# Performance work log

Hardware: AMD Instinct MI355X
Metric: run time of the kernel (lower is better)

Reference implementation:

```python
import jax, jax.numpy as jnp
import numpy as np

K = 10  # knn_graph default neighbors (self excluded)
NEG = 0.2  # LeakyReLU slope


def lrelu(x):
    return jnp.where(x > 0, x, NEG * x)


def conv1x1_1d(x, w):  # x: (B,Ci,N), w: (Co,Ci)
    return jnp.einsum('oi,bin->bon', w, x)


def conv1x1_2d(x, w):  # x: (B,Ci,N,k), w: (Co,Ci)
    return jnp.einsum('oi,bink->bonk', w, x)


def bn1(x, s, b):  # folded eval-mode BN, x: (B,C,N)
    return x * s[None, :, None] + b[None, :, None]


def bn2(x, s, b):  # x: (B,C,N,k)
    return x * s[None, :, None, None] + b[None, :, None, None]


def knn_graph(x, k=K):
    # x: (B, D, N) -> edge features (B, 2D, N, k)
    xt = jnp.transpose(x, (0, 2, 1))  # (B,N,D)
    sq = jnp.sum(xt * xt, axis=-1)  # (B,N)
    d2 = sq[:, :, None] + sq[:, None, :] - 2.0 * jnp.einsum('bnd,bmd->bnm', xt, xt)
    _, idx = jax.lax.top_k(-d2, k + 1)  # nearest k+1 incl. self
    idx = idx[:, :, 1:]  # drop self -> (B,N,k)
    B = xt.shape[0]
    feats = xt[jnp.arange(B)[:, None, None], idx]  # (B,N,k,D)
    center = xt[:, :, None, :]  # (B,N,1,D)
    edge = jnp.concatenate((feats - center, jnp.broadcast_to(center, feats.shape)), axis=-1)
    return jnp.transpose(edge, (0, 3, 1, 2))  # (B,2D,N,k)


def _make_params(key):
    ks = iter(jax.random.split(key, 32))
    def W(co, ci):
        return jax.random.normal(next(ks), (co, ci), jnp.float32) * (1.0 / np.sqrt(ci))
    def SB(c):
        return (jax.random.uniform(next(ks), (c,), jnp.float32, 0.5, 1.5),
                jax.random.normal(next(ks), (c,), jnp.float32) * 0.1)
    p = {}
    p['w1'] = W(64, 6);    p['s1'], p['b1'] = SB(64)
    p['w2'] = W(64, 64);   p['s2'], p['b2'] = SB(64)
    p['w3'] = W(64, 128);  p['s3'], p['b3'] = SB(64)
    p['w4'] = W(64, 64);   p['s4'], p['b4'] = SB(64)
    p['w5'] = W(64, 128);  p['s5'], p['b5'] = SB(64)
    p['w6'] = W(1024, 192); p['s6'], p['b6'] = SB(1024)
    p['w7'] = W(64, 16);   p['s7'], p['b7'] = SB(64)
    p['wp1'] = W(256, 1280); p['sp1'], p['bp1'] = SB(256)
    p['wp2'] = W(256, 256);  p['sp2'], p['bp2'] = SB(256)
    p['wp3'] = W(128, 256);  p['sp3'], p['bp3'] = SB(128)
    p['wp4'] = W(6, 128)
    return p


def setup_inputs() -> dict:
    key = jax.random.key(0)
    k0, k1, k2 = jax.random.split(key, 3)
    inp = {
        'points': jax.random.normal(k0, (8, 2048, 3), jnp.float32),
        'label': jax.random.uniform(k1, (8, 16), jnp.float32),
    }
    inp.update(_make_params(k2))
    return inp


def reference(points, label,
              w1, s1, b1, w2, s2, b2, w3, s3, b3, w4, s4, b4, w5, s5, b5,
              w6, s6, b6, w7, s7, b7,
              wp1, sp1, bp1, wp2, sp2, bp2, wp3, sp3, bp3, wp4):
    B, N, _ = points.shape
    x0 = jnp.transpose(points, (0, 2, 1))  # (B,3,N)

    e1 = knn_graph(x0)                                   # (B,6,N,k)
    h = lrelu(bn2(conv1x1_2d(e1, w1), s1, b1))
    out1 = jnp.max(lrelu(bn2(conv1x1_2d(h, w2), s2, b2)), axis=-1)  # (B,64,N)

    e2 = knn_graph(out1)                                 # (B,128,N,k)
    h = lrelu(bn2(conv1x1_2d(e2, w3), s3, b3))
    out2 = jnp.max(lrelu(bn2(conv1x1_2d(h, w4), s4, b4)), axis=-1)  # (B,64,N)

    e3 = knn_graph(out2)                                 # (B,128,N,k)
    out3 = jnp.max(lrelu(bn2(conv1x1_2d(e3, w5), s5, b5)), axis=-1)  # (B,64,N)

    comb = jnp.concatenate((out1, out2, out3), axis=1)   # (B,192,N)
    out4 = lrelu(bn1(conv1x1_1d(comb, w6), s6, b6))      # (B,1024,N)
    out4 = jnp.max(out4, axis=-1, keepdims=True)         # (B,1024,1)

    cat_vet = lrelu(bn1(conv1x1_1d(label[:, :, None], w7), s7, b7))  # (B,64,1)
    glob = jnp.broadcast_to(jnp.concatenate((out4, cat_vet), axis=1), (B, 1088, N))

    out = jnp.concatenate((out1, out2, out3, glob), axis=1)  # (B,1280,N)
    out = lrelu(bn1(conv1x1_1d(out, wp1), sp1, bp1))
    out = lrelu(bn1(conv1x1_1d(out, wp2), sp2, bp2))  # dropout = identity (eval)
    out = lrelu(bn1(conv1x1_1d(out, wp3), sp3, bp3))
    out = conv1x1_1d(out, wp4)                         # (B,6,N)
    return jnp.transpose(out, (0, 2, 1))               # (B,N,6)
```

## Files before the change

### kernel.cpp

```cpp
#include <hip/hip_runtime.h>
#include <float.h>

#define NEG 0.2f
constexpr int BATCH = 8;
constexpr int NPTS  = 2048;
constexpr int KNN   = 10;
constexpr int KP1   = 11;

__device__ __forceinline__ float lrelu(float x) { return x > 0.f ? x : NEG * x; }

__device__ __forceinline__ unsigned long long dkey(float d, int m) {
    unsigned u = __float_as_uint(d);
    u ^= (unsigned)((int)u >> 31) | 0x80000000u;
    return ((unsigned long long)u << 32) | (unsigned)m;
}

template<int D>
__global__ void sq_kernel(const float* __restrict__ xt, float* __restrict__ sq) {
    int i = blockIdx.x * 256 + threadIdx.x;
    if (i >= BATCH * NPTS) return;
    const float* p = xt + (size_t)i * D;
    float s = 0.f;
    #pragma unroll
    for (int d = 0; d < D; ++d) s += p[d] * p[d];
    sq[i] = s;
}

__global__ void sq64_kernel(const float* __restrict__ xt, float* __restrict__ sq) {
    int i = blockIdx.x * 256 + threadIdx.x;
    if (i >= BATCH * NPTS) return;
    const float4* p = (const float4*)(xt + (size_t)i * 64);
    float4 s4 = {0.f, 0.f, 0.f, 0.f};
    #pragma unroll
    for (int d = 0; d < 16; ++d) {
        float4 v = p[d];
        s4.x += v.x * v.x; s4.y += v.y * v.y; s4.z += v.z * v.z; s4.w += v.w * v.w;
    }
    sq[i] = (s4.x + s4.y) + (s4.z + s4.w);
}

template<int D>
__global__ __launch_bounds__(256) void knn_kernel(const float* __restrict__ xt,
                                                  const float* __restrict__ sq,
                                                  int* __restrict__ idx_out) {
    const int bn = blockIdx.x;
    const int b  = bn / NPTS;
    const int tid = threadIdx.x;

    __shared__ float xq[D];
    for (int i = tid; i < D; i += 256) xq[i] = xt[(size_t)bn * D + i];
    __syncthreads();

    const float sqn = sq[bn];
    const float* xb = xt + (size_t)b * NPTS * D;

    unsigned long long lk[KP1];
    #pragma unroll
    for (int j = 0; j < KP1; ++j) lk[j] = ~0ULL;

    for (int m = tid; m < NPTS; m += 256) {
        const float* xm = xb + (size_t)m * D;
        float dot = 0.f;
        #pragma unroll
        for (int i = 0; i < D; ++i) dot += xq[i] * xm[i];
        float cd = sqn + sq[b * NPTS + m] - 2.f * dot;
        unsigned long long key = dkey(cd, m);
        if (key < lk[KP1 - 1]) {
            #pragma unroll
            for (int j = 0; j < KP1; ++j) {
                bool better = key < lk[j];
                unsigned long long tk = lk[j];
                if (better) { lk[j] = key; key = tk; }
            }
        }
    }

    __shared__ unsigned long long sk[256 * KP1];
    #pragma unroll
    for (int j = 0; j < KP1; ++j) sk[tid * KP1 + j] = lk[j];
    __syncthreads();

    for (int step = 1; step < 256; step <<= 1) {
        if ((tid & (2 * step - 1)) == 0) {
            unsigned long long* ka = sk + tid * KP1;
            unsigned long long* kb = sk + (tid + step) * KP1;
            unsigned long long rk[KP1];
            int pa = 0, pb = 0;
            #pragma unroll
            for (int j = 0; j < KP1; ++j) {
                unsigned long long av = ka[pa], bv = kb[pb];
                bool takeA = av < bv;
                if (takeA) { rk[j] = av; ++pa; } else { rk[j] = bv; ++pb; }
            }
            #pragma unroll
            for (int j = 0; j < KP1; ++j) ka[j] = rk[j];
        }
        __syncthreads();
    }

    if (tid < KNN) idx_out[(size_t)bn * KNN + tid] = (int)(unsigned)(sk[tid + 1]);
}

__global__ __launch_bounds__(256) void knn64_kernel(const float* __restrict__ xt,
                                                    const float* __restrict__ sq,
                                                    int* __restrict__ idx_out) {
    const int t  = threadIdx.x;
    const int qg = t >> 5;
    const int lc = t & 31;
    const int bn0 = blockIdx.x * 8;
    const int bn  = bn0 + qg;
    const int b   = bn >> 11;
    const float* xb = xt + (size_t)b * NPTS * 64;

    __shared__ __align__(16) char smem[22528];
    float4 (*tile4)[16] = reinterpret_cast<float4(*)[16]>(smem);
    unsigned long long* sk = reinterpret_cast<unsigned long long*>(smem);

    float4 xq[16];
    {
        const float4* xqp = (const float4*)(xt + (size_t)bn * 64);
        #pragma unroll
        for (int i = 0; i < 16; ++i) xq[i] = xqp[i];
    }
    const float sqn = sq[bn];
    const float* sqb_ = sq + b * NPTS;

    unsigned long long lk[KP1];
    #pragma unroll
    for (int j = 0; j < KP1; ++j) lk[j] = ~0ULL;

    const int ci  = t >> 3;
    const int sub = t & 7;

    for (int t0 = 0; t0 < NPTS; t0 += 32) {
        __syncthreads();
        {
            const float4* src = (const float4*)(xb + (size_t)(t0 + ci) * 64 + sub * 8);
            float4 u0 = src[0], u1 = src[1];
            tile4[ci][(2 * sub)     ^ (ci & 15)] = u0;
            tile4[ci][(2 * sub + 1) ^ (ci & 15)] = u1;
        }
        __syncthreads();

        const int m = t0 + lc;
        float a0 = 0.f, a1 = 0.f, a2 = 0.f, a3 = 0.f;
        #pragma unroll
        for (int i = 0; i < 16; ++i) {
            float4 v = tile4[lc][i ^ (lc & 15)];
            a0 += xq[i].x * v.x;
            a1 += xq[i].y * v.y;
            a2 += xq[i].z * v.z;
            a3 += xq[i].w * v.w;
        }
        float dot = (a0 + a1) + (a2 + a3);
        float cd = sqn + sqb_[m] - 2.f * dot;
        unsigned long long key = dkey(cd, m);
        if (key < lk[KP1 - 1]) {
            #pragma unroll
            for (int j = 0; j < KP1; ++j) {
                bool better = key < lk[j];
                unsigned long long tk = lk[j];
                if (better) { lk[j] = key; key = tk; }
            }
        }
    }

    __syncthreads();
    #pragma unroll
    for (int j = 0; j < KP1; ++j) sk[t * KP1 + j] = lk[j];
    __syncthreads();

    for (int step = 1; step < 32; step <<= 1) {
        if ((lc & (2 * step - 1)) == 0) {
            unsigned long long* ka = sk + t * KP1;
            unsigned long long* kb = sk + (t + step) * KP1;
            unsigned long long rk[KP1];
            int pa = 0, pb = 0;
            #pragma unroll
            for (int j = 0; j < KP1; ++j) {
                unsigned long long av = ka[pa], bv = kb[pb];
                bool takeA = av < bv;
                if (takeA) { rk[j] = av; ++pa; } else { rk[j] = bv; ++pb; }
            }
            #pragma unroll
            for (int j = 0; j < KP1; ++j) ka[j] = rk[j];
        }
        __syncthreads();
    }

    if (lc < KNN) idx_out[(size_t)bn * KNN + lc] = (int)(unsigned)(sk[(qg * 32) * KP1 + lc + 1]);
}

__global__ __launch_bounds__(64) void edgeconv1_kernel(
    const float* __restrict__ pts, const int* __restrict__ idx,
    const float* __restrict__ w1, const float* __restrict__ s1, const float* __restrict__ b1,
    const float* __restrict__ w2, const float* __restrict__ s2, const float* __restrict__ b2,
    float* __restrict__ outt) {
    const int bn = blockIdx.x;
    const int b  = bn / NPTS;
    const int c  = threadIdx.x;

    const float cx = pts[bn * 3 + 0], cy = pts[bn * 3 + 1], cz = pts[bn * 3 + 2];

    float w1r[6];
    #pragma unroll
    for (int i = 0; i < 6; ++i) w1r[i] = w1[c * 6 + i];
    const float s1c = s1[c], b1c = b1[c], s2c = s2[c], b2c = b2[c];

    __shared__ float h1all[KNN][64];
    #pragma unroll
    for (int k = 0; k < KNN; ++k) {
        const int m = idx[bn * KNN + k];
        const float* f = pts + ((size_t)b * NPTS + m) * 3;
        const float e0 = f[0] - cx, e1 = f[1] - cy, e2 = f[2] - cz;
        float a = w1r[0] * e0 + w1r[1] * e1 + w1r[2] * e2
                + w1r[3] * cx + w1r[4] * cy + w1r[5] * cz;
        h1all[k][c] = lrelu(a * s1c + b1c);
    }
    __syncthreads();

    float a2[KNN];
    #pragma unroll
    for (int k = 0; k < KNN; ++k) a2[k] = 0.f;
    for (int j4 = 0; j4 < 16; ++j4) {
        float4 wv = *(const float4*)&w2[c * 64 + j4 * 4];
        #pragma unroll
        for (int k = 0; k < KNN; ++k) {
            float4 h4 = *(const float4*)&h1all[k][j4 * 4];
            a2[k] += wv.x * h4.x + wv.y * h4.y + wv.z * h4.z + wv.w * h4.w;
        }
    }
    float mx = -FLT_MAX;
    #pragma unroll
    for (int k = 0; k < KNN; ++k) mx = fmaxf(mx, lrelu(a2[k] * s2c + b2c));
    outt[(size_t)bn * 64 + c] = mx;
}

__global__ __launch_bounds__(64) void edgeconv2_kernel(
    const float* __restrict__ xin, const int* __restrict__ idx,
    const float* __restrict__ w3, const float* __restrict__ s3, const float* __restrict__ b3,
    const float* __restrict__ w4, const float* __restrict__ s4, const float* __restrict__ b4,
    float* __restrict__ outt) {
    const int bn = blockIdx.x;
    const int b  = bn / NPTS;
    const int c  = threadIdx.x;

    __shared__ float cen[64];
    __shared__ float fea[KNN][64];
    __shared__ float h1all[KNN][64];
    cen[c] = xin[(size_t)bn * 64 + c];
    #pragma unroll
    for (int k = 0; k < KNN; ++k) {
        const int m = idx[bn * KNN + k];
        fea[k][c] = xin[((size_t)b * NPTS + m) * 64 + c];
    }
    __syncthreads();

    float a[KNN];
    #pragma unroll
    for (int k = 0; k < KNN; ++k) a[k] = 0.f;
    float4 ab = {0.f, 0.f, 0.f, 0.f};
    for (int j4 = 0; j4 < 16; ++j4) {
        float4 wa = *(const float4*)&w3[c * 128 + j4 * 4];
        float4 wb = *(const float4*)&w3[c * 128 + 64 + j4 * 4];
        float4 c4 = *(const float4*)&cen[j4 * 4];
        ab.x += (wb.x - wa.x) * c4.x; ab.y += (wb.y - wa.y) * c4.y;
        ab.z += (wb.z - wa.z) * c4.z; ab.w += (wb.w - wa.w) * c4.w;
        #pragma unroll
        for (int k = 0; k < KNN; ++k) {
            float4 f4 = *(const float4*)&fea[k][j4 * 4];
            a[k] += wa.x * f4.x + wa.y * f4.y + wa.z * f4.z + wa.w * f4.w;
        }
    }
    const float abase = (ab.x + ab.y) + (ab.z + ab.w);
    const float s3c = s3[c], b3c = b3[c], s4c = s4[c], b4c = b4[c];
    #pragma unroll
    for (int k = 0; k < KNN; ++k) h1all[k][c] = lrelu((a[k] + abase) * s3c + b3c);
    __syncthreads();

    float a2[KNN];
    #pragma unroll
    for (int k = 0; k < KNN; ++k) a2[k] = 0.f;
    for (int j4 = 0; j4 < 16; ++j4) {
        float4 wv = *(const float4*)&w4[c * 64 + j4 * 4];
        #pragma unroll
        for (int k = 0; k < KNN; ++k) {
            float4 h4 = *(const float4*)&h1all[k][j4 * 4];
            a2[k] += wv.x * h4.x + wv.y * h4.y + wv.z * h4.z + wv.w * h4.w;
        }
    }
    float mx = -FLT_MAX;
    #pragma unroll
    for (int k = 0; k < KNN; ++k) mx = fmaxf(mx, lrelu(a2[k] * s4c + b4c));
    outt[(size_t)bn * 64 + c] = mx;
}

__global__ __launch_bounds__(64) void edgeconv3_kernel(
    const float* __restrict__ xin, const int* __restrict__ idx,
    const float* __restrict__ w5, const float* __restrict__ s5, const float* __restrict__ b5,
    float* __restrict__ outt) {
    const int bn = blockIdx.x;
    const int b  = bn / NPTS;
    const int c  = threadIdx.x;

    __shared__ float cen[64];
    __shared__ float fea[KNN][64];
    cen[c] = xin[(size_t)bn * 64 + c];
    #pragma unroll
    for (int k = 0; k < KNN; ++k) {
        const int m = idx[bn * KNN + k];
        fea[k][c] = xin[((size_t)b * NPTS + m) * 64 + c];
    }
    __syncthreads();

    float a[KNN];
    #pragma unroll
    for (int k = 0; k < KNN; ++k) a[k] = 0.f;
    float4 ab = {0.f, 0.f, 0.f, 0.f};
    for (int j4 = 0; j4 < 16; ++j4) {
        float4 wa = *(const float4*)&w5[c * 128 + j4 * 4];
        float4 wb = *(const float4*)&w5[c * 128 + 64 + j4 * 4];
        float4 c4 = *(const float4*)&cen[j4 * 4];
        ab.x += (wb.x - wa.x) * c4.x; ab.y += (wb.y - wa.y) * c4.y;
        ab.z += (wb.z - wa.z) * c4.z; ab.w += (wb.w - wa.w) * c4.w;
        #pragma unroll
        for (int k = 0; k < KNN; ++k) {
            float4 f4 = *(const float4*)&fea[k][j4 * 4];
            a[k] += wa.x * f4.x + wa.y * f4.y + wa.z * f4.z + wa.w * f4.w;
        }
    }
    const float abase = (ab.x + ab.y) + (ab.z + ab.w);
    const float s5c = s5[c], b5c = b5[c];
    float mx = -FLT_MAX;
    #pragma unroll
    for (int k = 0; k < KNN; ++k) mx = fmaxf(mx, lrelu((a[k] + abase) * s5c + b5c));
    outt[(size_t)bn * 64 + c] = mx;
}

__global__ __launch_bounds__(64) void catvet_kernel(
    const float* __restrict__ label,
    const float* __restrict__ w7, const float* __restrict__ s7, const float* __restrict__ b7,
    float* __restrict__ catv) {
    const int b = blockIdx.x, c = threadIdx.x;
    float a = 0.f;
    #pragma unroll
    for (int i = 0; i < 16; ++i) a += w7[c * 16 + i] * label[b * 16 + i];
    catv[b * 64 + c] = lrelu(a * s7[c] + b7[c]);
}

__global__ void w6t_kernel(const float* __restrict__ w6, float* __restrict__ w6t) {
    int i = blockIdx.x * 256 + threadIdx.x;
    if (i >= 192 * 1024) return;
    int k = i >> 10, c = i & 1023;
    w6t[i] = w6[c * 192 + k];
}

constexpr int OPTS = 32;
__global__ __launch_bounds__(256) void out4max_kernel(
    const float* __restrict__ out1t, const float* __restrict__ out2t, const float* __restrict__ out3t,
    const float* __restrict__ w6t, float* __restrict__ partial) {
    const int blk = blockIdx.x;
    const int b   = blk >> 6;
    const int nt  = blk & 63;
    const int t   = threadIdx.x;

    __shared__ float xs[192 * OPTS];
    for (int idx = t; idx < 192 * OPTS; idx += 256) {
        int p = idx / 192, r = idx - p * 192;
        const size_t gp = (size_t)b * NPTS + nt * OPTS + p;
        float val;
        if (r < 64)       val = out1t[gp * 64 + r];
        else if (r < 128) val = out2t[gp * 64 + (r - 64)];
        else              val = out3t[gp * 64 + (r - 128)];
        xs[r * OPTS + p] = val;
    }
    __syncthreads();

    float mx0 = -FLT_MAX, mx1 = -FLT_MAX, mx2 = -FLT_MAX, mx3 = -FLT_MAX;
    #pragma unroll
    for (int pg = 0; pg < OPTS / 16; ++pg) {
        float acc0[16], acc1[16], acc2[16], acc3[16];
        #pragma unroll
        for (int p = 0; p < 16; ++p) { acc0[p] = 0.f; acc1[p] = 0.f; acc2[p] = 0.f; acc3[p] = 0.f; }
        #pragma unroll 2
        for (int k = 0; k < 192; ++k) {
            float4 wv = *(const float4*)&w6t[(size_t)k * 1024 + t * 4];
            const float4* xr4 = (const float4*)&xs[k * OPTS + pg * 16];
            #pragma unroll
            for (int p4 = 0; p4 < 4; ++p4) {
                float4 xv = xr4[p4];
                acc0[p4 * 4 + 0] += wv.x * xv.x; acc0[p4 * 4 + 1] += wv.x * xv.y;
                acc0[p4 * 4 + 2] += wv.x * xv.z; acc0[p4 * 4 + 3] += wv.x * xv.w;
                acc1[p4 * 4 + 0] += wv.y * xv.x; acc1[p4 * 4 + 1] += wv.y * xv.y;
                acc1[p4 * 4 + 2] += wv.y * xv.z; acc1[p4 * 4 + 3] += wv.y * xv.w;
                acc2[p4 * 4 + 0] += wv.z * xv.x; acc2[p4 * 4 + 1] += wv.z * xv.y;
                acc2[p4 * 4 + 2] += wv.z * xv.z; acc2[p4 * 4 + 3] += wv.z * xv.w;
                acc3[p4 * 4 + 0] += wv.w * xv.x; acc3[p4 * 4 + 1] += wv.w * xv.y;
                acc3[p4 * 4 + 2] += wv.w * xv.z; acc3[p4 * 4 + 3] += wv.w * xv.w;
            }
        }
        #pragma unroll
        for (int p = 0; p < 16; ++p) {
            mx0 = fmaxf(mx0, acc0[p]); mx1 = fmaxf(mx1, acc1[p]);
            mx2 = fmaxf(mx2, acc2[p]); mx3 = fmaxf(mx3, acc3[p]);
        }
    }
    float4 o = {mx0, mx1, mx2, mx3};
    *(float4*)&partial[(size_t)blk * 1024 + t * 4] = o;
}

__global__ __launch_bounds__(256) void out4reduce_kernel(
    const float* __restrict__ partial,
    const float* __restrict__ s6, const float* __restrict__ b6,
    float* __restrict__ out4m) {
    const int i = blockIdx.x * 256 + threadIdx.x;
    const int b = i >> 10, c = i & 1023;
    float m = -FLT_MAX;
    for (int nt = 0; nt < 64; ++nt)
        m = fmaxf(m, partial[((size_t)b * 64 + nt) * 1024 + c]);
    out4m[i] = lrelu(m * s6[c] + b6[c]);
}

__global__ __launch_bounds__(256) void gbias_kernel(
    const float* __restrict__ out4m, const float* __restrict__ catv,
    const float* __restrict__ wp1, float* __restrict__ g) {
    const int b = blockIdx.x, t = threadIdx.x;
    __shared__ float v[1088];
    for (int i = t; i < 1088; i += 256)
        v[i] = (i < 1024) ? out4m[(size_t)b * 1024 + i] : catv[(size_t)b * 64 + (i - 1024)];
    __syncthreads();
    const float* w = wp1 + (size_t)t * 1280 + 192;
    float4 s4 = {0.f, 0.f, 0.f, 0.f};
    for (int i = 0; i < 272; ++i) {
        float4 wv = *(const float4*)&w[i * 4];
        float4 vv = *(const float4*)&v[i * 4];
        s4.x += wv.x * vv.x; s4.y += wv.y * vv.y; s4.z += wv.z * vv.z; s4.w += wv.w * vv.w;
    }
    g[(size_t)b * 256 + t] = (s4.x + s4.y) + (s4.z + s4.w);
}

constexpr int HP = 16;
constexpr int KC = 16;

__global__ __launch_bounds__(256) void head_kernel(
    const float* __restrict__ out1t, const float* __restrict__ out2t, const float* __restrict__ out3t,
    const float* __restrict__ g,
    const float* __restrict__ wp1, const float* __restrict__ sp1, const float* __restrict__ bp1,
    const float* __restrict__ wp2, const float* __restrict__ sp2, const float* __restrict__ bp2,
    const float* __restrict__ wp3, const float* __restrict__ sp3, const float* __restrict__ bp3,
    const float* __restrict__ wp4, float* __restrict__ out) {
    const int p0 = blockIdx.x * HP;
    const int b  = p0 >> 11;
    const int t  = threadIdx.x;

    __shared__ float smA[4096];
    __shared__ float smB[4096];
    __shared__ float smW[KC * 256];

    for (int e = t; e < 192 * HP; e += 256) {
        int p = e / 192, k = e - p * 192;
        float val;
        if (k < 64)       val = out1t[((size_t)(p0 + p)) * 64 + k];
        else if (k < 128) val = out2t[((size_t)(p0 + p)) * 64 + (k - 64)];
        else              val = out3t[((size_t)(p0 + p)) * 64 + (k - 128)];
        smA[k * HP + p] = val;
    }

    const int og = t & 31;
    const int pg = t >> 5;

    float acc[2][8];
    #pragma unroll
    for (int i = 0; i < 8; ++i) {
        float gv = g[(size_t)b * 256 + og * 8 + i];
        acc[0][i] = gv; acc[1][i] = gv;
    }
    for (int kc = 0; kc < 192 / KC; ++kc) {
        __syncthreads();
        #pragma unroll
        for (int it = 0; it < KC; ++it)
            smW[it * 256 + t] = wp1[(size_t)t * 1280 + kc * KC + it];
        __syncthreads();
        #pragma unroll 4
        for (int kk = 0; kk < KC; ++kk) {
            int k = kc * KC + kk;
            float2 xv = *(const float2*)&smA[k * HP + pg * 2];
            float4 w0 = *(const float4*)&smW[kk * 256 + og * 8];
            float4 w1v = *(const float4*)&smW[kk * 256 + og * 8 + 4];
            float wv[8] = {w0.x, w0.y, w0.z, w0.w, w1v.x, w1v.y, w1v.z, w1v.w};
            #pragma unroll
            for (int i = 0; i < 8; ++i) {
                acc[0][i] += xv.x * wv[i];
                acc[1][i] += xv.y * wv[i];
            }
        }
    }
    #pragma unroll
    for (int i = 0; i < 8; ++i) {
        int o = og * 8 + i;
        float sc = sp1[o], bc = bp1[o];
        smB[o * HP + pg * 2 + 0] = lrelu(acc[0][i] * sc + bc);
        smB[o * HP + pg * 2 + 1] = lrelu(acc[1][i] * sc + bc);
    }

    float acc2[2][8];
    #pragma unroll
    for (int i = 0; i < 8; ++i) { acc2[0][i] = 0.f; acc2[1][i] = 0.f; }
    for (int kc = 0; kc < 256 / KC; ++kc) {
        __syncthreads();
        #pragma unroll
        for (int it = 0; it < KC; ++it)
            smW[it * 256 + t] = wp2[(size_t)t * 256 + kc * KC + it];
        __syncthreads();
        #pragma unroll 4
        for (int kk = 0; kk < KC; ++kk) {
            int k = kc * KC + kk;
            float2 xv = *(const float2*)&smB[k * HP + pg * 2];
            float4 w0 = *(const float4*)&smW[kk * 256 + og * 8];
            float4 w1v = *(const float4*)&smW[kk * 256 + og * 8 + 4];
            float wv[8] = {w0.x, w0.y, w0.z, w0.w, w1v.x, w1v.y, w1v.z, w1v.w};
            #pragma unroll
            for (int i = 0; i < 8; ++i) {
                acc2[0][i] += xv.x * wv[i];
                acc2[1][i] += xv.y * wv[i];
            }
        }
    }
    __syncthreads();
    #pragma unroll
    for (int i = 0; i < 8; ++i) {
        int o = og * 8 + i;
        float sc = sp2[o], bc = bp2[o];
        smA[o * HP + pg * 2 + 0] = lrelu(acc2[0][i] * sc + bc);
        smA[o * HP + pg * 2 + 1] = lrelu(acc2[1][i] * sc + bc);
    }

    const int og3 = t & 15;
    const int p3  = t >> 4;
    float acc3[8];
    #pragma unroll
    for (int i = 0; i < 8; ++i) acc3[i] = 0.f;
    for (int kc = 0; kc < 256 / KC; ++kc) {
        __syncthreads();
        for (int e = t; e < KC * 128; e += 256) {
            int kk = e >> 7, o = e & 127;
            smW[kk * 128 + o] = wp3[(size_t)o * 256 + kc * KC + kk];
        }
        __syncthreads();
        #pragma unroll 4
        for (int kk = 0; kk < KC; ++kk) {
            int k = kc * KC + kk;
            float xv = smA[k * HP + p3];
            float4 w0 = *(const float4*)&smW[kk * 128 + og3 * 8];
            float4 w1v = *(const float4*)&smW[kk * 128 + og3 * 8 + 4];
            float wv[8] = {w0.x, w0.y, w0.z, w0.w, w1v.x, w1v.y, w1v.z, w1v.w};
            #pragma unroll
            for (int i = 0; i < 8; ++i) acc3[i] += xv * wv[i];
        }
    }
    __syncthreads();
    #pragma unroll
    for (int i = 0; i < 8; ++i) {
        int o = og3 * 8 + i;
        float sc = sp3[o], bc = bp3[o];
        smB[o * HP + p3] = lrelu(acc3[i] * sc + bc);
    }
    __syncthreads();

    if (t < HP * 6) {
        int p = t / 6, o = t - p * 6;
        float4 s4 = {0.f, 0.f, 0.f, 0.f};
        for (int k4 = 0; k4 < 32; ++k4) {
            float4 wv = *(const float4*)&wp4[o * 128 + k4 * 4];
            s4.x += wv.x * smB[(k4 * 4 + 0) * HP + p];
            s4.y += wv.y * smB[(k4 * 4 + 1) * HP + p];
            s4.z += wv.z * smB[(k4 * 4 + 2) * HP + p];
            s4.w += wv.w * smB[(k4 * 4 + 3) * HP + p];
        }
        out[((size_t)(p0 + p)) * 6 + o] = (s4.x + s4.y) + (s4.z + s4.w);
    }
}

extern "C" void kernel_launch(void* const* d_in, const int* in_sizes, int n_in,
                              void* d_out, int out_size, void* d_ws, size_t ws_size,
                              hipStream_t stream) {
    const float* points = (const float*)d_in[0];
    const float* label  = (const float*)d_in[1];
    const float* w1  = (const float*)d_in[2];
    const float* s1  = (const float*)d_in[3];
    const float* b1  = (const float*)d_in[4];
    const float* w2  = (const float*)d_in[5];
    const float* s2  = (const float*)d_in[6];
    const float* b2  = (const float*)d_in[7];
    const float* w3  = (const float*)d_in[8];
    const float* s3  = (const float*)d_in[9];
    const float* b3  = (const float*)d_in[10];
    const float* w4  = (const float*)d_in[11];
    const float* s4  = (const float*)d_in[12];
    const float* b4  = (const float*)d_in[13];
    const float* w5  = (const float*)d_in[14];
    const float* s5  = (const float*)d_in[15];
    const float* b5  = (const float*)d_in[16];
    const float* w6  = (const float*)d_in[17];
    const float* s6  = (const float*)d_in[18];
    const float* b6  = (const float*)d_in[19];
    const float* w7  = (const float*)d_in[20];
    const float* s7  = (const float*)d_in[21];
    const float* b7  = (const float*)d_in[22];
    const float* wp1 = (const float*)d_in[23];
    const float* sp1 = (const float*)d_in[24];
    const float* bp1 = (const float*)d_in[25];
    const float* wp2 = (const float*)d_in[26];
    const float* sp2 = (const float*)d_in[27];
    const float* bp2 = (const float*)d_in[28];
    const float* wp3 = (const float*)d_in[29];
    const float* sp3 = (const float*)d_in[30];
    const float* bp3 = (const float*)d_in[31];
    const float* wp4 = (const float*)d_in[32];

    float* ws = (float*)d_ws;
    size_t off = 0;
    auto alloc = [&](size_t nf) { float* p = ws + off; off += nf; return p; };
    float* out1t = alloc((size_t)BATCH * NPTS * 64);
    float* out2t = alloc((size_t)BATCH * NPTS * 64);
    float* out3t = alloc((size_t)BATCH * NPTS * 64);
    float* sqb   = alloc((size_t)BATCH * NPTS);
    float* out4m = alloc((size_t)BATCH * 1024);
    float* catv  = alloc((size_t)BATCH * 64);
    float* gb    = alloc((size_t)BATCH * 256);
    float* w6t   = alloc((size_t)192 * 1024);
    float* part  = alloc((size_t)512 * 1024);
    int* idx1 = (int*)alloc((size_t)BATCH * NPTS * KNN);
    int* idx2 = (int*)alloc((size_t)BATCH * NPTS * KNN);
    int* idx3 = (int*)alloc((size_t)BATCH * NPTS * KNN);

    const int BN = BATCH * NPTS;
    const int sqBlocks = (BN + 255) / 256;

    sq_kernel<3><<<sqBlocks, 256, 0, stream>>>(points, sqb);
    knn_kernel<3><<<BN, 256, 0, stream>>>(points, sqb, idx1);
    edgeconv1_kernel<<<BN, 64, 0, stream>>>(points, idx1, w1, s1, b1, w2, s2, b2, out1t);

    sq64_kernel<<<sqBlocks, 256, 0, stream>>>(out1t, sqb);
    knn64_kernel<<<BN / 8, 256, 0, stream>>>(out1t, sqb, idx2);
    edgeconv2_kernel<<<BN, 64, 0, stream>>>(out1t, idx2, w3, s3, b3, w4, s4, b4, out2t);

    sq64_kernel<<<sqBlocks, 256, 0, stream>>>(out2t, sqb);
    knn64_kernel<<<BN / 8, 256, 0, stream>>>(out2t, sqb, idx3);
    edgeconv3_kernel<<<BN, 64, 0, stream>>>(out2t, idx3, w5, s5, b5, out3t);

    catvet_kernel<<<BATCH, 64, 0, stream>>>(label, w7, s7, b7, catv);
    w6t_kernel<<<(192 * 1024 + 255) / 256, 256, 0, stream>>>(w6, w6t);
    out4max_kernel<<<512, 256, 0, stream>>>(out1t, out2t, out3t, w6t, part);
    out4reduce_kernel<<<BATCH * 1024 / 256, 256, 0, stream>>>(part, s6, b6, out4m);
    gbias_kernel<<<BATCH, 256, 0, stream>>>(out4m, catv, wp1, gb);

    head_kernel<<<BN / HP, 256, 0, stream>>>(out1t, out2t, out3t, gb,
                                             wp1, sp1, bp1, wp2, sp2, bp2, wp3, sp3, bp3,
                                             wp4, (float*)d_out);
}
```

Measured before the change: 1.154 ms.

## Replace shared-memory merge trees in kNN with wavefront shuffle top-k selection

The 3-D kNN kernel now runs one 64-lane wavefront per query instead of 256 threads, and the final top-k selection in both kNN kernels uses repeated shuffle-xor min reductions instead of a shared-memory pairwise merge tree with block barriers. Each of the 11 rounds finds the global minimum key and pops it from the owning lane's sorted list. This removes the large shared-memory buffer and the many __syncthreads, and it frees LDS in knn64 for higher occupancy. In exchange each lane scans more candidates in the 3-D kernel, and every round adds 64-bit shuffle reductions.

```diff
diff --git a/kernel.cpp b/kernel.cpp
--- a/kernel.cpp
+++ b/kernel.cpp
@@ -39,31 +39,30 @@
     sq[i] = (s4.x + s4.y) + (s4.z + s4.w);
 }
 
-template<int D>
-__global__ __launch_bounds__(256) void knn_kernel(const float* __restrict__ xt,
+__global__ __launch_bounds__(64) void knn3_kernel(const float* __restrict__ xt,
                                                   const float* __restrict__ sq,
                                                   int* __restrict__ idx_out) {
     const int bn = blockIdx.x;
-    const int b  = bn / NPTS;
-    const int tid = threadIdx.x;
-
-    __shared__ float xq[D];
-    for (int i = tid; i < D; i += 256) xq[i] = xt[(size_t)bn * D + i];
-    __syncthreads();
-
+    const int b  = bn >> 11;
+    const int l  = threadIdx.x;
+
+    const float qx = xt[(size_t)bn * 3 + 0];
+    const float qy = xt[(size_t)bn * 3 + 1];
+    const float qz = xt[(size_t)bn * 3 + 2];
     const float sqn = sq[bn];
-    const float* xb = xt + (size_t)b * NPTS * D;
+    const float* xb  = xt + (size_t)b * NPTS * 3;
+    const float* sqb_ = sq + (size_t)b * NPTS;
 
     unsigned long long lk[KP1];
     #pragma unroll
     for (int j = 0; j < KP1; ++j) lk[j] = ~0ULL;
 
-    for (int m = tid; m < NPTS; m += 256) {
-        const float* xm = xb + (size_t)m * D;
+    for (int m = l; m < NPTS; m += 64) {
         float dot = 0.f;
-        #pragma unroll
-        for (int i = 0; i < D; ++i) dot += xq[i] * xm[i];
-        float cd = sqn + sq[b * NPTS + m] - 2.f * dot;
+        dot += qx * xb[m * 3 + 0];
+        dot += qy * xb[m * 3 + 1];
+        dot += qz * xb[m * 3 + 2];
+        float cd = sqn + sqb_[m] - 2.f * dot;
         unsigned long long key = dkey(cd, m);
         if (key < lk[KP1 - 1]) {
             #pragma unroll
@@ -75,30 +74,22 @@
         }
     }
 
-    __shared__ unsigned long long sk[256 * KP1];
-    #pragma unroll
-    for (int j = 0; j < KP1; ++j) sk[tid * KP1 + j] = lk[j];
-    __syncthreads();
-
-    for (int step = 1; step < 256; step <<= 1) {
-        if ((tid & (2 * step - 1)) == 0) {
-            unsigned long long* ka = sk + tid * KP1;
-            unsigned long long* kb = sk + (tid + step) * KP1;
-            unsigned long long rk[KP1];
-            int pa = 0, pb = 0;
-            #pragma unroll
-            for (int j = 0; j < KP1; ++j) {
-                unsigned long long av = ka[pa], bv = kb[pb];
-                bool takeA = av < bv;
-                if (takeA) { rk[j] = av; ++pa; } else { rk[j] = bv; ++pb; }
-            }
-            #pragma unroll
-            for (int j = 0; j < KP1; ++j) ka[j] = rk[j];
-        }
-        __syncthreads();
-    }
-
-    if (tid < KNN) idx_out[(size_t)bn * KNN + tid] = (int)(unsigned)(sk[tid + 1]);
+    #pragma unroll
+    for (int k = 0; k < KP1; ++k) {
+        unsigned long long mk = lk[0];
+        #pragma unroll
+        for (int s = 32; s >= 1; s >>= 1) {
+            unsigned long long o = __shfl_xor(mk, s, 64);
+            mk = (o < mk) ? o : mk;
+        }
+        if (k >= 1 && l == k - 1)
+            idx_out[(size_t)bn * KNN + (k - 1)] = (int)(unsigned)mk;
+        if (lk[0] == mk) {
+            #pragma unroll
+            for (int j = 0; j < KP1 - 1; ++j) lk[j] = lk[j + 1];
+            lk[KP1 - 1] = ~0ULL;
+        }
+    }
 }
 
 __global__ __launch_bounds__(256) void knn64_kernel(const float* __restrict__ xt,
@@ -112,9 +103,7 @@
     const int b   = bn >> 11;
     const float* xb = xt + (size_t)b * NPTS * 64;
 
-    __shared__ __align__(16) char smem[22528];
-    float4 (*tile4)[16] = reinterpret_cast<float4(*)[16]>(smem);
-    unsigned long long* sk = reinterpret_cast<unsigned long long*>(smem);
+    __shared__ __align__(16) float4 tile4[32][16];
 
     float4 xq[16];
     {
@@ -165,30 +154,22 @@
         }
     }
 
-    __syncthreads();
-    #pragma unroll
-    for (int j = 0; j < KP1; ++j) sk[t * KP1 + j] = lk[j];
-    __syncthreads();
-
-    for (int step = 1; step < 32; step <<= 1) {
-        if ((lc & (2 * step - 1)) == 0) {
-            unsigned long long* ka = sk + t * KP1;
-            unsigned long long* kb = sk + (t + step) * KP1;
-            unsigned long long rk[KP1];
-            int pa = 0, pb = 0;
-            #pragma unroll
-            for (int j = 0; j < KP1; ++j) {
-                unsigned long long av = ka[pa], bv = kb[pb];
-                bool takeA = av < bv;
-                if (takeA) { rk[j] = av; ++pa; } else { rk[j] = bv; ++pb; }
-            }
-            #pragma unroll
-            for (int j = 0; j < KP1; ++j) ka[j] = rk[j];
-        }
-        __syncthreads();
-    }
-
-    if (lc < KNN) idx_out[(size_t)bn * KNN + lc] = (int)(unsigned)(sk[(qg * 32) * KP1 + lc + 1]);
+    #pragma unroll
+    for (int k = 0; k < KP1; ++k) {
+        unsigned long long mk = lk[0];
+        #pragma unroll
+        for (int s = 16; s >= 1; s >>= 1) {
+            unsigned long long o = __shfl_xor(mk, s, 32);
+            mk = (o < mk) ? o : mk;
+        }
+        if (k >= 1 && lc == k - 1)
+            idx_out[(size_t)bn * KNN + (k - 1)] = (int)(unsigned)mk;
+        if (lk[0] == mk) {
+            #pragma unroll
+            for (int j = 0; j < KP1 - 1; ++j) lk[j] = lk[j + 1];
+            lk[KP1 - 1] = ~0ULL;
+        }
+    }
 }
 
 __global__ __launch_bounds__(64) void edgeconv1_kernel(
@@ -638,7 +619,7 @@
     const int sqBlocks = (BN + 255) / 256;
 
     sq_kernel<3><<<sqBlocks, 256, 0, stream>>>(points, sqb);
-    knn_kernel<3><<<BN, 256, 0, stream>>>(points, sqb, idx1);
+    knn3_kernel<<<BN, 64, 0, stream>>>(points, sqb, idx1);
     edgeconv1_kernel<<<BN, 64, 0, stream>>>(points, idx1, w1, s1, b1, w2, s2, b2, out1t);
 
     sq64_kernel<<<sqBlocks, 256, 0, stream>>>(out1t, sqb);
```

After: 1.116 ms. -3.3%, faster.
